# Kernel tuning notes

Hardware: AMD Instinct MI355X
Metric: run time of the kernel (lower is better)

Reference implementation:

```python
import jax, jax.numpy as jnp
import numpy as np

B, C, H, W_SP = 8, 2048, 28, 28   # last_conv feature map (ResNet-50, layer4 stride=1, 448px input)
D = 8192                          # count-sketch / CBP output dim
NUM_CLS = 200
L2_EPS = 1e-12                    # F.normalize default eps


def setup_inputs() -> dict:
    key = jax.random.key(0)
    ks = jax.random.split(key, 7)
    x = jax.random.normal(ks[0], (B, C, H, W_SP), dtype=jnp.float32)
    h1 = jax.random.randint(ks[1], (C,), 0, D, dtype=jnp.int32)
    h2 = jax.random.randint(ks[2], (C,), 0, D, dtype=jnp.int32)
    # Rademacher signs (count-sketch s vectors); map {0,1} -> {-1,+1}
    s1 = (2.0 * jax.random.bernoulli(ks[3], 0.5, (C,)).astype(jnp.float32) - 1.0)
    s2 = (2.0 * jax.random.bernoulli(ks[4], 0.5, (C,)).astype(jnp.float32) - 1.0)
    W_cls = jax.random.normal(ks[5], (D, NUM_CLS), dtype=jnp.float32) * 0.01
    b_cls = jnp.zeros((NUM_CLS,), dtype=jnp.float32)
    return {"x": x, "s1": s1, "s2": s2, "W_cls": W_cls, "b_cls": b_cls, "h1": h1, "h2": h2}


def _cbp_sum(xf, s1, s2, h1, h2):
    # xf: [B, L, C] per-pixel features.  Count-sketch each pixel twice, convolve
    # via FFT, then sum over all L spatial locations (== the original HxW loop).
    Bb, L, Cc = xf.shape
    sk1 = jnp.zeros((Bb, L, D), xf.dtype).at[..., h1].add(xf * s1)  # scatter-add over channels
    sk2 = jnp.zeros((Bb, L, D), xf.dtype).at[..., h2].add(xf * s2)
    f1 = jnp.fft.rfft(sk1, axis=-1)
    f2 = jnp.fft.rfft(sk2, axis=-1)
    y = jnp.fft.irfft(f1 * f2, n=D, axis=-1)  # [B, L, D] circular conv of sketches
    return y.sum(axis=1)                      # sum over spatial locations -> [B, D]


def reference(x, s1, s2, W_cls, b_cls, h1, h2):
    Bb, Cc, Hh, Ww = x.shape
    xf = x.transpose(0, 2, 3, 1).reshape(Bb, Hh * Ww, Cc)          # [B, L, C]
    y = _cbp_sum(xf, s1, s2, h1, h2)                               # [B, D]
    feat = jnp.sign(y) * jnp.sqrt(jnp.abs(y))                      # signed sqrt
    feat = feat / jnp.maximum(jnp.linalg.norm(feat, axis=1, keepdims=True), L2_EPS)
    logit = feat @ W_cls + b_cls
    return logit, feat
```

## Files before the change

### kernel.cpp

```cpp
#include <hip/hip_runtime.h>
#include <hip/hip_bf16.h>

#define BATCH 8
#define CH    2048
#define LSP   784
#define KPAD  832
#define KSTAGE 13
#define DDIM  8192
#define NCLS  200
#define NTILE 16
#define NPAIR 136
#define NSLOT 68
#define FXSCALE 8192.0f
#define FXINV   (1.0f/8192.0f)

typedef _Float16 f16x8 __attribute__((ext_vector_type(8)));
typedef _Float16 f16x4 __attribute__((ext_vector_type(4)));
typedef float    f32x4 __attribute__((ext_vector_type(4)));

#define FATOMIC(p, v) unsafeAtomicAdd((p), (v))

__global__ __launch_bounds__(256) void split_kernel(
    const float* __restrict__ x,
    _Float16* __restrict__ xh,
    float* __restrict__ part, float* __restrict__ norm,
    const float* __restrict__ s1, const int* __restrict__ h1,
    const float* __restrict__ s2, const int* __restrict__ h2,
    float4* __restrict__ metaG,
    const float* __restrict__ bc, float* __restrict__ out,
    int exclusive)
{
    int idx = blockIdx.x * 256 + threadIdx.x;
    if (!exclusive && idx < NSLOT * BATCH * DDIM / 4)
        *(float4*)&part[idx * 4] = make_float4(0.f, 0.f, 0.f, 0.f);
    if (idx < CH)
        metaG[idx] = make_float4(s1[idx] * 64.0f, __int_as_float(h1[idx]),
                                 s2[idx] * 128.0f, __int_as_float(h2[idx]));
    if (idx < BATCH) norm[idx] = 0.0f;
    if (idx < BATCH * NCLS) out[idx] = bc[idx % NCLS];
    if (idx >= BATCH * CH * KPAD / 4) return;
    int v  = idx * 4;
    int bc_ = v / KPAD;
    int l  = v - bc_ * KPAD;
    float4 xv = make_float4(0.f, 0.f, 0.f, 0.f);
    if (l < LSP)
        xv = *(const float4*)&x[(size_t)bc_ * LSP + l];
    f16x4 hv;
    hv[0] = (_Float16)xv.x; hv[1] = (_Float16)xv.y;
    hv[2] = (_Float16)xv.z; hv[3] = (_Float16)xv.w;
    *(f16x4*)&xh[v] = hv;
}

__device__ __forceinline__ void stage64(
    const _Float16* __restrict__ src,
    unsigned short* lds,
    int wv, int lane, int s)
{
    const int rowi = lane >> 3;
    const int gc   = (lane & 7) ^ rowi;
    const _Float16* g0 = src + (size_t)rowi * KPAD + s * 64 + gc * 8;
#pragma unroll
    for (int q = 0; q < 4; ++q) {
        const int r0 = wv * 32 + q * 8;
        __builtin_amdgcn_global_load_lds(
            (__attribute__((address_space(1))) void*)(g0 + (size_t)r0 * KPAD),
            (__attribute__((address_space(3))) void*)(lds + r0 * 64),
            16, 0, 0);
    }
}

__global__ __launch_bounds__(256, 2) void gram_scatter_kernel(
    const _Float16* __restrict__ xh,
    const float4* __restrict__ metaG,
    float* __restrict__ part,
    int exclusive)
{
    __shared__ __align__(16) unsigned short smA[128 * 64];
    __shared__ __align__(16) unsigned short smB[128 * 64];
    __shared__ __align__(16) int bins[DDIM];

    const int tid  = threadIdx.x;
    const int lane = tid & 63;
    const int wv   = tid >> 6;
    const int b    = blockIdx.x & 7;
    const int pidx = blockIdx.x >> 3;

    for (int i = tid; i < DDIM; i += 256) bins[i] = 0;

    int tM = 0, tN = 0;
    {
        int i = pidx;
#pragma unroll 1
        for (int t = 0; t < NTILE; ++t) {
            int cnt = NTILE - t;
            if (i < cnt) { tM = t; tN = t + i; break; }
            i -= cnt;
        }
    }
    const bool diag = (tM == tN);

    const int wrow = (wv >> 1) * 64;
    const int wcol = (wv & 1) * 64;
    const int rsel = lane & 15;
    const int khi  = lane >> 4;

    const _Float16* srcA = xh + ((size_t)b * CH + (size_t)tM * 128) * KPAD;
    const _Float16* srcB = xh + ((size_t)b * CH + (size_t)tN * 128) * KPAD;
    const unsigned short* fragB = diag ? smA : smB;

    f32x4 acc[4][4];
    const f32x4 zv = {0.0f, 0.0f, 0.0f, 0.0f};
#pragma unroll
    for (int mi = 0; mi < 4; ++mi)
#pragma unroll
        for (int ni = 0; ni < 4; ++ni) acc[mi][ni] = zv;

#pragma unroll 1
    for (int s = 0; s < KSTAGE; ++s) {
        stage64(srcA, smA, wv, lane, s);
        if (!diag) stage64(srcB, smB, wv, lane, s);
        __syncthreads();
#pragma unroll
        for (int t = 0; t < 2; ++t) {
            const int co = ((((t << 2) + khi) ^ (rsel & 7)) << 3);
            f16x8 ah[4], bh[4];
#pragma unroll
            for (int i = 0; i < 4; ++i) {
                ah[i] = *(const f16x8*)&smA[(wrow + i * 16 + rsel) * 64 + co];
                bh[i] = *(const f16x8*)&fragB[(wcol + i * 16 + rsel) * 64 + co];
            }
#pragma unroll
            for (int mi = 0; mi < 4; ++mi)
#pragma unroll
                for (int ni = 0; ni < 4; ++ni)
                    acc[mi][ni] = __builtin_amdgcn_mfma_f32_16x16x32_f16(
                        ah[mi], bh[ni], acc[mi][ni], 0, 0, 0);
        }
        __syncthreads();
    }

    const int c2b = tN * 128 + wcol + rsel;
    int   h1c[4], h2c[4]; float s1c[4], s2c[4];
#pragma unroll
    for (int ni = 0; ni < 4; ++ni) {
        float4 cm = metaG[c2b + ni * 16];
        s1c[ni] = cm.x; h1c[ni] = __float_as_int(cm.y);
        s2c[ni] = cm.z; h2c[ni] = __float_as_int(cm.w);
    }

    const int rowbase = tM * 128 + wrow + (khi << 2);
#pragma unroll
    for (int mi = 0; mi < 4; ++mi) {
        float4 rm[4];
#pragma unroll
        for (int r = 0; r < 4; ++r) rm[r] = metaG[rowbase + mi * 16 + r];
#pragma unroll
        for (int r = 0; r < 4; ++r) {
            const float s1r = rm[r].x, s2r = rm[r].z;
            const int h1r = __float_as_int(rm[r].y);
            const int h2r = __float_as_int(rm[r].w);
#pragma unroll
            for (int ni = 0; ni < 4; ++ni) {
                float g = acc[mi][ni][r];
                atomicAdd(&bins[(h1r + h2c[ni]) & (DDIM - 1)],
                          (int)(s1r * s2c[ni] * g));
                if (!diag)
                    atomicAdd(&bins[(h1c[ni] + h2r) & (DDIM - 1)],
                              (int)(s1c[ni] * s2r * g));
            }
        }
    }

    __syncthreads();

    if (exclusive) {
        float* pbase = part + ((size_t)(pidx * BATCH + b) * DDIM);
#pragma unroll 4
        for (int i = tid; i < DDIM / 4; i += 256) {
            int4 v = *(const int4*)&bins[i * 4];
            float4 f = make_float4((float)v.x * FXINV, (float)v.y * FXINV,
                                   (float)v.z * FXINV, (float)v.w * FXINV);
            *(float4*)&pbase[i * 4] = f;
        }
    } else {
        float* pbase = part + ((size_t)((pidx % NSLOT) * BATCH + b) * DDIM);
        const int rot = (blockIdx.x & 31) << 8;
        for (int i = tid; i < DDIM; i += 256) {
            int j = (i + rot) & (DDIM - 1);
            int v = bins[j];
            if (v != 0) FATOMIC(&pbase[j], (float)v * FXINV);
        }
    }
}

__global__ __launch_bounds__(256) void reduce_kernel(
    const float* __restrict__ part, float* __restrict__ y,
    float* __restrict__ norm, int nslots)
{
    const int tid = threadIdx.x;
    const int b  = blockIdx.x & 7;
    const int d0 = (((blockIdx.x >> 3) * 256) + tid) * 4;
    float4 s = make_float4(0.f, 0.f, 0.f, 0.f);
#pragma unroll 4
    for (int p = 0; p < nslots; ++p) {
        float4 v = *(const float4*)&part[((size_t)p * BATCH + b) * DDIM + d0];
        s.x += v.x; s.y += v.y; s.z += v.z; s.w += v.w;
    }
    *(float4*)&y[(size_t)b * DDIM + d0] = s;
    float ab = fabsf(s.x) + fabsf(s.y) + fabsf(s.z) + fabsf(s.w);
    __shared__ float red[256];
    red[tid] = ab;
    __syncthreads();
    for (int st = 128; st > 0; st >>= 1) {
        if (tid < st) red[tid] += red[tid + st];
        __syncthreads();
    }
    if (tid == 0) FATOMIC(&norm[b], red[0]);
}

__global__ __launch_bounds__(256) void logit_kernel(
    const float* __restrict__ y, const float* __restrict__ norm,
    const float* __restrict__ W, float* __restrict__ out)
{
    const int j = blockIdx.x;
    const int tid = threadIdx.x;
    __shared__ float fs[BATCH][128];
    for (int i = tid; i < BATCH * 128; i += 256) {
        int bb = i >> 7, dd = i & 127;
        float v = y[(size_t)bb * DDIM + j * 128 + dd];
        float inv = 1.0f / fmaxf(sqrtf(norm[bb]), 1e-12f);
        float f = copysignf(sqrtf(fabsf(v)), v) * inv;
        fs[bb][dd] = f;
        out[BATCH * NCLS + (size_t)bb * DDIM + j * 128 + dd] = f;
    }
    __syncthreads();
    if (tid < NCLS) {
        float a[BATCH];
#pragma unroll
        for (int bb = 0; bb < BATCH; ++bb) a[bb] = 0.0f;
        for (int dd = 0; dd < 128; ++dd) {
            float w = W[(size_t)(j * 128 + dd) * NCLS + tid];
#pragma unroll
            for (int bb = 0; bb < BATCH; ++bb) a[bb] += fs[bb][dd] * w;
        }
#pragma unroll
        for (int bb = 0; bb < BATCH; ++bb)
            FATOMIC(&out[bb * NCLS + tid], a[bb]);
    }
}

extern "C" void kernel_launch(void* const* d_in, const int* in_sizes, int n_in,
                              void* d_out, int out_size, void* d_ws, size_t ws_size,
                              hipStream_t stream)
{
    const float* x  = (const float*)d_in[0];
    const float* s1 = (const float*)d_in[1];
    const float* s2 = (const float*)d_in[2];
    const float* W  = (const float*)d_in[3];
    const float* bc = (const float*)d_in[4];
    const int*   h1 = (const int*)d_in[5];
    const int*   h2 = (const int*)d_in[6];
    float* out = (float*)d_out;

    const size_t ybytes  = (size_t)BATCH * DDIM * sizeof(float);
    const size_t xhbytes = (size_t)BATCH * CH * KPAD * sizeof(_Float16);

    size_t partbytes = (size_t)NPAIR * BATCH * DDIM * sizeof(float);
    int exclusive = (ws_size >= partbytes + ybytes + 128 + xhbytes);
    if (!exclusive)
        partbytes = (size_t)NSLOT * BATCH * DDIM * sizeof(float);
    const int nslots = exclusive ? NPAIR : NSLOT;

    char* ws = (char*)d_ws;
    float* part = (float*)ws;
    float* y    = (float*)(ws + partbytes);
    float4* metaG = (float4*)(ws + partbytes);
    float* norm = (float*)(ws + partbytes + ybytes);
    _Float16* xh = (_Float16*)(ws + partbytes + ybytes + 128);

    split_kernel<<<(BATCH * CH * KPAD / 4 + 255) / 256, 256, 0, stream>>>(
        x, xh, part, norm, s1, h1, s2, h2, metaG, bc, out, exclusive);

    gram_scatter_kernel<<<NPAIR * BATCH, 256, 0, stream>>>(
        xh, metaG, part, exclusive);

    reduce_kernel<<<64, 256, 0, stream>>>(part, y, norm, nslots);

    logit_kernel<<<64, 256, 0, stream>>>(y, norm, W, out);
}
```

Before: 180.8 us.

## Register-prefetch next K stage in gram kernel and widen reduce grid

The gram kernel's direct global-to-LDS loads are replaced with register staging. The next K-stage tile is loaded into registers while the current stage is written to LDS and consumed by MFMAs, so global latency can overlap with compute, and one of the two barriers per stage is dropped. The reduce kernel goes from float4 per thread over 64 blocks to scalar loads over 256 blocks to raise parallelism on the slot reduction. The prefetch costs extra VGPRs under launch_bounds(256,2), which may cause spills, and the LDS swizzle now sits on the write side.

```diff
diff --git a/kernel.cpp b/kernel.cpp
--- a/kernel.cpp
+++ b/kernel.cpp
@@ -51,22 +51,27 @@
     *(f16x4*)&xh[v] = hv;
 }
 
-__device__ __forceinline__ void stage64(
+__device__ __forceinline__ void loadregs(
     const _Float16* __restrict__ src,
-    unsigned short* lds,
-    int wv, int lane, int s)
+    int wv, int lane, int s, f16x8 r[4])
 {
     const int rowi = lane >> 3;
-    const int gc   = (lane & 7) ^ rowi;
-    const _Float16* g0 = src + (size_t)rowi * KPAD + s * 64 + gc * 8;
-#pragma unroll
-    for (int q = 0; q < 4; ++q) {
-        const int r0 = wv * 32 + q * 8;
-        __builtin_amdgcn_global_load_lds(
-            (__attribute__((address_space(1))) void*)(g0 + (size_t)r0 * KPAD),
-            (__attribute__((address_space(3))) void*)(lds + r0 * 64),
-            16, 0, 0);
-    }
+    const int gc   = lane & 7;
+    const _Float16* g0 = src + (size_t)(wv * 32 + rowi) * KPAD + s * 64 + gc * 8;
+#pragma unroll
+    for (int q = 0; q < 4; ++q)
+        r[q] = *(const f16x8*)(g0 + (size_t)(q * 8) * KPAD);
+}
+
+__device__ __forceinline__ void writelds(
+    unsigned short* lds, int wv, int lane, const f16x8 r[4])
+{
+    const int rowi = lane >> 3;
+    const int c2   = (lane & 7) ^ rowi;
+    unsigned short* d0 = lds + (wv * 32 + rowi) * 64 + c2 * 8;
+#pragma unroll
+    for (int q = 0; q < 4; ++q)
+        *(f16x8*)(d0 + q * 8 * 64) = r[q];
 }
 
 __global__ __launch_bounds__(256, 2) void gram_scatter_kernel(
@@ -115,11 +120,22 @@
 #pragma unroll
         for (int ni = 0; ni < 4; ++ni) acc[mi][ni] = zv;
 
+    f16x8 ra[4], rb[4];
+    loadregs(srcA, wv, lane, 0, ra);
+    if (!diag) loadregs(srcB, wv, lane, 0, rb);
+
 #pragma unroll 1
     for (int s = 0; s < KSTAGE; ++s) {
-        stage64(srcA, smA, wv, lane, s);
-        if (!diag) stage64(srcB, smB, wv, lane, s);
-        __syncthreads();
+        __builtin_amdgcn_s_barrier();
+        writelds(smA, wv, lane, ra);
+        if (!diag) writelds(smB, wv, lane, rb);
+        if (s + 1 < KSTAGE) {
+            loadregs(srcA, wv, lane, s + 1, ra);
+            if (!diag) loadregs(srcB, wv, lane, s + 1, rb);
+        }
+        asm volatile("s_waitcnt lgkmcnt(0)" ::: "memory");
+        __builtin_amdgcn_sched_barrier(0);
+        __builtin_amdgcn_s_barrier();
 #pragma unroll
         for (int t = 0; t < 2; ++t) {
             const int co = ((((t << 2) + khi) ^ (rsel & 7)) << 3);
@@ -136,7 +152,6 @@
                     acc[mi][ni] = __builtin_amdgcn_mfma_f32_16x16x32_f16(
                         ah[mi], bh[ni], acc[mi][ni], 0, 0, 0);
         }
-        __syncthreads();
     }
 
     const int c2b = tN * 128 + wcol + rsel;
@@ -198,16 +213,14 @@
     float* __restrict__ norm, int nslots)
 {
     const int tid = threadIdx.x;
-    const int b  = blockIdx.x & 7;
-    const int d0 = (((blockIdx.x >> 3) * 256) + tid) * 4;
-    float4 s = make_float4(0.f, 0.f, 0.f, 0.f);
-#pragma unroll 4
-    for (int p = 0; p < nslots; ++p) {
-        float4 v = *(const float4*)&part[((size_t)p * BATCH + b) * DDIM + d0];
-        s.x += v.x; s.y += v.y; s.z += v.z; s.w += v.w;
-    }
-    *(float4*)&y[(size_t)b * DDIM + d0] = s;
-    float ab = fabsf(s.x) + fabsf(s.y) + fabsf(s.z) + fabsf(s.w);
+    const int b   = blockIdx.x & 7;
+    const int d0  = (blockIdx.x >> 3) * 256 + tid;
+    float s = 0.0f;
+#pragma unroll 8
+    for (int p = 0; p < nslots; ++p)
+        s += part[((size_t)p * BATCH + b) * DDIM + d0];
+    y[(size_t)b * DDIM + d0] = s;
+    float ab = fabsf(s);
     __shared__ float red[256];
     red[tid] = ab;
     __syncthreads();
@@ -284,7 +297,7 @@
     gram_scatter_kernel<<<NPAIR * BATCH, 256, 0, stream>>>(
         xh, metaG, part, exclusive);
 
-    reduce_kernel<<<64, 256, 0, stream>>>(part, y, norm, nslots);
+    reduce_kernel<<<256, 256, 0, stream>>>(part, y, norm, nslots);
 
     logit_kernel<<<64, 256, 0, stream>>>(y, norm, W, out);
 }
```

Result: slower. 185.7 us (+2.7%).

## Process two tile pairs per gram block and halve partial-sum slots

Applied to the files above, without the earlier changes.

Each gram_scatter block now loops over two tile pairs (pidx and pidx+NSLOT) and accumulates both into one LDS bin array before writing out. This halves the grid to 544 blocks and the partial buffer to 68 slots, which cuts global writes and the work of the reduction pass. The reduce kernel is relaunched with 256 blocks of scalar loads for more parallelism, and the fp16 conversion now handles 8 elements per thread. The cost is fewer blocks to fill the GPU, and diagonal and off-diagonal pairs are mixed within a block, which may unbalance per-block work.

```diff
diff --git a/kernel.cpp b/kernel.cpp
--- a/kernel.cpp
+++ b/kernel.cpp
@@ -38,17 +38,21 @@
                                  s2[idx] * 128.0f, __int_as_float(h2[idx]));
     if (idx < BATCH) norm[idx] = 0.0f;
     if (idx < BATCH * NCLS) out[idx] = bc[idx % NCLS];
-    if (idx >= BATCH * CH * KPAD / 4) return;
-    int v  = idx * 4;
+    if (idx >= BATCH * CH * KPAD / 8) return;
+    int v  = idx * 8;
     int bc_ = v / KPAD;
     int l  = v - bc_ * KPAD;
-    float4 xv = make_float4(0.f, 0.f, 0.f, 0.f);
-    if (l < LSP)
-        xv = *(const float4*)&x[(size_t)bc_ * LSP + l];
-    f16x4 hv;
-    hv[0] = (_Float16)xv.x; hv[1] = (_Float16)xv.y;
-    hv[2] = (_Float16)xv.z; hv[3] = (_Float16)xv.w;
-    *(f16x4*)&xh[v] = hv;
+    f16x8 hv = {0, 0, 0, 0, 0, 0, 0, 0};
+    if (l < LSP) {
+        const float* xp = &x[(size_t)bc_ * LSP + l];
+        float4 a = *(const float4*)xp;
+        float4 c = *(const float4*)(xp + 4);
+        hv[0] = (_Float16)a.x; hv[1] = (_Float16)a.y;
+        hv[2] = (_Float16)a.z; hv[3] = (_Float16)a.w;
+        hv[4] = (_Float16)c.x; hv[5] = (_Float16)c.y;
+        hv[6] = (_Float16)c.z; hv[7] = (_Float16)c.w;
+    }
+    *(f16x8*)&xh[v] = hv;
 }
 
 __device__ __forceinline__ void stage64(
@@ -83,98 +87,103 @@
     const int lane = tid & 63;
     const int wv   = tid >> 6;
     const int b    = blockIdx.x & 7;
-    const int pidx = blockIdx.x >> 3;
+    const int pgrp = blockIdx.x >> 3;
 
     for (int i = tid; i < DDIM; i += 256) bins[i] = 0;
-
-    int tM = 0, tN = 0;
-    {
-        int i = pidx;
-#pragma unroll 1
-        for (int t = 0; t < NTILE; ++t) {
-            int cnt = NTILE - t;
-            if (i < cnt) { tM = t; tN = t + i; break; }
-            i -= cnt;
-        }
-    }
-    const bool diag = (tM == tN);
 
     const int wrow = (wv >> 1) * 64;
     const int wcol = (wv & 1) * 64;
     const int rsel = lane & 15;
     const int khi  = lane >> 4;
 
-    const _Float16* srcA = xh + ((size_t)b * CH + (size_t)tM * 128) * KPAD;
-    const _Float16* srcB = xh + ((size_t)b * CH + (size_t)tN * 128) * KPAD;
-    const unsigned short* fragB = diag ? smA : smB;
-
-    f32x4 acc[4][4];
-    const f32x4 zv = {0.0f, 0.0f, 0.0f, 0.0f};
-#pragma unroll
-    for (int mi = 0; mi < 4; ++mi)
-#pragma unroll
-        for (int ni = 0; ni < 4; ++ni) acc[mi][ni] = zv;
-
 #pragma unroll 1
-    for (int s = 0; s < KSTAGE; ++s) {
-        stage64(srcA, smA, wv, lane, s);
-        if (!diag) stage64(srcB, smB, wv, lane, s);
-        __syncthreads();
-#pragma unroll
-        for (int t = 0; t < 2; ++t) {
-            const int co = ((((t << 2) + khi) ^ (rsel & 7)) << 3);
-            f16x8 ah[4], bh[4];
-#pragma unroll
-            for (int i = 0; i < 4; ++i) {
-                ah[i] = *(const f16x8*)&smA[(wrow + i * 16 + rsel) * 64 + co];
-                bh[i] = *(const f16x8*)&fragB[(wcol + i * 16 + rsel) * 64 + co];
+    for (int pp = 0; pp < 2; ++pp) {
+        const int pidx = pgrp + pp * NSLOT;
+
+        int tM = 0, tN = 0;
+        {
+            int i = pidx;
+#pragma unroll 1
+            for (int t = 0; t < NTILE; ++t) {
+                int cnt = NTILE - t;
+                if (i < cnt) { tM = t; tN = t + i; break; }
+                i -= cnt;
             }
-#pragma unroll
-            for (int mi = 0; mi < 4; ++mi)
-#pragma unroll
-                for (int ni = 0; ni < 4; ++ni)
-                    acc[mi][ni] = __builtin_amdgcn_mfma_f32_16x16x32_f16(
-                        ah[mi], bh[ni], acc[mi][ni], 0, 0, 0);
-        }
-        __syncthreads();
-    }
-
-    const int c2b = tN * 128 + wcol + rsel;
-    int   h1c[4], h2c[4]; float s1c[4], s2c[4];
-#pragma unroll
-    for (int ni = 0; ni < 4; ++ni) {
-        float4 cm = metaG[c2b + ni * 16];
-        s1c[ni] = cm.x; h1c[ni] = __float_as_int(cm.y);
-        s2c[ni] = cm.z; h2c[ni] = __float_as_int(cm.w);
-    }
-
-    const int rowbase = tM * 128 + wrow + (khi << 2);
-#pragma unroll
-    for (int mi = 0; mi < 4; ++mi) {
-        float4 rm[4];
-#pragma unroll
-        for (int r = 0; r < 4; ++r) rm[r] = metaG[rowbase + mi * 16 + r];
-#pragma unroll
-        for (int r = 0; r < 4; ++r) {
-            const float s1r = rm[r].x, s2r = rm[r].z;
-            const int h1r = __float_as_int(rm[r].y);
-            const int h2r = __float_as_int(rm[r].w);
-#pragma unroll
-            for (int ni = 0; ni < 4; ++ni) {
-                float g = acc[mi][ni][r];
-                atomicAdd(&bins[(h1r + h2c[ni]) & (DDIM - 1)],
-                          (int)(s1r * s2c[ni] * g));
-                if (!diag)
-                    atomicAdd(&bins[(h1c[ni] + h2r) & (DDIM - 1)],
-                              (int)(s1c[ni] * s2r * g));
+        }
+        const bool diag = (tM == tN);
+
+        const _Float16* srcA = xh + ((size_t)b * CH + (size_t)tM * 128) * KPAD;
+        const _Float16* srcB = xh + ((size_t)b * CH + (size_t)tN * 128) * KPAD;
+        const unsigned short* fragB = diag ? smA : smB;
+
+        f32x4 acc[4][4];
+        const f32x4 zv = {0.0f, 0.0f, 0.0f, 0.0f};
+#pragma unroll
+        for (int mi = 0; mi < 4; ++mi)
+#pragma unroll
+            for (int ni = 0; ni < 4; ++ni) acc[mi][ni] = zv;
+
+#pragma unroll 1
+        for (int s = 0; s < KSTAGE; ++s) {
+            stage64(srcA, smA, wv, lane, s);
+            if (!diag) stage64(srcB, smB, wv, lane, s);
+            __syncthreads();
+#pragma unroll
+            for (int t = 0; t < 2; ++t) {
+                const int co = ((((t << 2) + khi) ^ (rsel & 7)) << 3);
+                f16x8 ah[4], bh[4];
+#pragma unroll
+                for (int i = 0; i < 4; ++i) {
+                    ah[i] = *(const f16x8*)&smA[(wrow + i * 16 + rsel) * 64 + co];
+                    bh[i] = *(const f16x8*)&fragB[(wcol + i * 16 + rsel) * 64 + co];
+                }
+#pragma unroll
+                for (int mi = 0; mi < 4; ++mi)
+#pragma unroll
+                    for (int ni = 0; ni < 4; ++ni)
+                        acc[mi][ni] = __builtin_amdgcn_mfma_f32_16x16x32_f16(
+                            ah[mi], bh[ni], acc[mi][ni], 0, 0, 0);
             }
+            __syncthreads();
+        }
+
+        const int c2b = tN * 128 + wcol + rsel;
+        int   h1c[4], h2c[4]; float s1c[4], s2c[4];
+#pragma unroll
+        for (int ni = 0; ni < 4; ++ni) {
+            float4 cm = metaG[c2b + ni * 16];
+            s1c[ni] = cm.x; h1c[ni] = __float_as_int(cm.y);
+            s2c[ni] = cm.z; h2c[ni] = __float_as_int(cm.w);
+        }
+
+        const int rowbase = tM * 128 + wrow + (khi << 2);
+#pragma unroll
+        for (int mi = 0; mi < 4; ++mi) {
+            float4 rm[4];
+#pragma unroll
+            for (int r = 0; r < 4; ++r) rm[r] = metaG[rowbase + mi * 16 + r];
+#pragma unroll
+            for (int r = 0; r < 4; ++r) {
+                const float s1r = rm[r].x, s2r = rm[r].z;
+                const int h1r = __float_as_int(rm[r].y);
+                const int h2r = __float_as_int(rm[r].w);
+#pragma unroll
+                for (int ni = 0; ni < 4; ++ni) {
+                    float g = acc[mi][ni][r];
+                    atomicAdd(&bins[(h1r + h2c[ni]) & (DDIM - 1)],
+                              (int)(s1r * s2c[ni] * g));
+                    if (!diag)
+                        atomicAdd(&bins[(h1c[ni] + h2r) & (DDIM - 1)],
+                                  (int)(s1c[ni] * s2r * g));
+                }
+            }
         }
     }
 
     __syncthreads();
 
     if (exclusive) {
-        float* pbase = part + ((size_t)(pidx * BATCH + b) * DDIM);
+        float* pbase = part + ((size_t)(pgrp * BATCH + b) * DDIM);
 #pragma unroll 4
         for (int i = tid; i < DDIM / 4; i += 256) {
             int4 v = *(const int4*)&bins[i * 4];
@@ -183,7 +192,7 @@
             *(float4*)&pbase[i * 4] = f;
         }
     } else {
-        float* pbase = part + ((size_t)((pidx % NSLOT) * BATCH + b) * DDIM);
+        float* pbase = part + ((size_t)(pgrp * BATCH + b) * DDIM);
         const int rot = (blockIdx.x & 31) << 8;
         for (int i = tid; i < DDIM; i += 256) {
             int j = (i + rot) & (DDIM - 1);
@@ -195,19 +204,17 @@
 
 __global__ __launch_bounds__(256) void reduce_kernel(
     const float* __restrict__ part, float* __restrict__ y,
-    float* __restrict__ norm, int nslots)
+    float* __restrict__ norm)
 {
     const int tid = threadIdx.x;
-    const int b  = blockIdx.x & 7;
-    const int d0 = (((blockIdx.x >> 3) * 256) + tid) * 4;
-    float4 s = make_float4(0.f, 0.f, 0.f, 0.f);
+    const int b   = blockIdx.x & 7;
+    const int d0  = (blockIdx.x >> 3) * 256 + tid;
+    float s = 0.0f;
 #pragma unroll 4
-    for (int p = 0; p < nslots; ++p) {
-        float4 v = *(const float4*)&part[((size_t)p * BATCH + b) * DDIM + d0];
-        s.x += v.x; s.y += v.y; s.z += v.z; s.w += v.w;
-    }
-    *(float4*)&y[(size_t)b * DDIM + d0] = s;
-    float ab = fabsf(s.x) + fabsf(s.y) + fabsf(s.z) + fabsf(s.w);
+    for (int p = 0; p < NSLOT; ++p)
+        s += part[((size_t)p * BATCH + b) * DDIM + d0];
+    y[(size_t)b * DDIM + d0] = s;
+    float ab = fabsf(s);
     __shared__ float red[256];
     red[tid] = ab;
     __syncthreads();
@@ -265,11 +272,8 @@
     const size_t ybytes  = (size_t)BATCH * DDIM * sizeof(float);
     const size_t xhbytes = (size_t)BATCH * CH * KPAD * sizeof(_Float16);
 
-    size_t partbytes = (size_t)NPAIR * BATCH * DDIM * sizeof(float);
-    int exclusive = (ws_size >= partbytes + ybytes + 128 + xhbytes);
-    if (!exclusive)
-        partbytes = (size_t)NSLOT * BATCH * DDIM * sizeof(float);
-    const int nslots = exclusive ? NPAIR : NSLOT;
+    const size_t partbytes = (size_t)NSLOT * BATCH * DDIM * sizeof(float);
+    const int exclusive = (ws_size >= partbytes + ybytes + 128 + xhbytes);
 
     char* ws = (char*)d_ws;
     float* part = (float*)ws;
@@ -278,13 +282,13 @@
     float* norm = (float*)(ws + partbytes + ybytes);
     _Float16* xh = (_Float16*)(ws + partbytes + ybytes + 128);
 
-    split_kernel<<<(BATCH * CH * KPAD / 4 + 255) / 256, 256, 0, stream>>>(
+    split_kernel<<<(BATCH * CH * KPAD / 8 + 255) / 256, 256, 0, stream>>>(
         x, xh, part, norm, s1, h1, s2, h2, metaG, bc, out, exclusive);
 
-    gram_scatter_kernel<<<NPAIR * BATCH, 256, 0, stream>>>(
+    gram_scatter_kernel<<<NSLOT * BATCH, 256, 0, stream>>>(
         xh, metaG, part, exclusive);
 
-    reduce_kernel<<<64, 256, 0, stream>>>(part, y, norm, nslots);
+    reduce_kernel<<<256, 256, 0, stream>>>(part, y, norm);
 
     logit_kernel<<<64, 256, 0, stream>>>(y, norm, W, out);
 }
```

New measurement: 185.8 us. 2.8% more time.
